# Optimization experiments

Measured on AMD Instinct MI355X. Metric: run time of the kernel, lower is better.

Reference implementation:

```python
import jax, jax.numpy as jnp
import numpy as np

SCORE_THRESHOLD = 0.5
IOU_THRESHOLD = 0.5
N = 8192
IMG = 640.0


def setup_inputs() -> dict:
    key = jax.random.key(0)
    k1, k2, k3 = jax.random.split(key, 3)
    # valid xyxy boxes on a 640px canvas: x2 > x1, y2 > y1
    xy1 = jax.random.uniform(k1, (N, 2), dtype=jnp.float32) * (IMG - 64.0)
    wh = jax.random.uniform(k2, (N, 2), dtype=jnp.float32) * 96.0 + 4.0
    xyxy = jnp.concatenate([xy1, xy1 + wh], axis=1)  # [N,4]
    person_conf = jax.random.uniform(k3, (N,), dtype=jnp.float32)  # [N]
    return {"xyxy": xyxy, "person_conf": person_conf}


def _pairwise_iou(boxes):
    # boxes: [N,4] xyxy -> iou: [N,N]
    x1, y1, x2, y2 = boxes[:, 0], boxes[:, 1], boxes[:, 2], boxes[:, 3]
    area = (x2 - x1) * (y2 - y1)  # [N]
    ix1 = jnp.maximum(x1[:, None], x1[None, :])
    iy1 = jnp.maximum(y1[:, None], y1[None, :])
    ix2 = jnp.minimum(x2[:, None], x2[None, :])
    iy2 = jnp.minimum(y2[:, None], y2[None, :])
    iw = jnp.maximum(ix2 - ix1, 0.0)
    ih = jnp.maximum(iy2 - iy1, 0.0)
    inter = iw * ih
    union = area[:, None] + area[None, :] - inter
    return inter / jnp.maximum(union, 1e-9)


def reference(xyxy, person_conf):
    # score-threshold filter (as a mask to stay jit-compatible / fixed shape)
    valid = person_conf >= SCORE_THRESHOLD  # [N]
    # sort by score descending; invalid boxes sink to the bottom
    sort_scores = jnp.where(valid, person_conf, -jnp.inf)
    order = jnp.argsort(-sort_scores)  # [N]
    boxes_s = xyxy[order]              # [N,4]
    scores_s = person_conf[order]      # [N]
    valid_s = valid[order]             # [N]

    iou = _pairwise_iou(boxes_s)  # [N,N]
    idx = jnp.arange(N)

    def body(i, keep):
        # box i (if still kept) suppresses lower-scored overlapping boxes
        sup = keep[i] & (iou[i] > IOU_THRESHOLD) & (idx > i)
        return keep & ~sup

    keep = jax.lax.fori_loop(0, N, body, valid_s)  # [N] bool

    boxes_and_scores = jnp.concatenate([boxes_s, scores_s[:, None]], axis=1)  # [N,5]
    out = jnp.where(keep[:, None], boxes_and_scores, 0.0)  # suppressed rows zeroed
    return out, keep
```

## Files before the change

kernel.cpp:

```cpp
#include <hip/hip_runtime.h>

typedef unsigned long long u64;
typedef unsigned int u32;

static constexpr int N = 8192;
static constexpr int NW = N / 64;
static constexpr int CAPE = 12288;
static constexpr int EPT = CAPE / 1024;


__device__ __forceinline__ u64 make_key(float s, int i) {
  u32 adj = (s >= 0.5f) ? (__float_as_uint(s) + 1u) : 0u;
  return ((u64)adj << 32) | (u64)(u32)(N - 1 - i);
}

__global__ __launch_bounds__(256)
void rank_kernel(const float* __restrict__ conf, u32* __restrict__ rank_partial) {
  __shared__ u64 sk[1024];
  const int t = threadIdx.x;
  const int jb = blockIdx.y;
  for (int k = t; k < 1024; k += 256) {
    int j = jb * 1024 + k;
    sk[k] = make_key(conf[j], j);
  }
  __syncthreads();
  const int i = blockIdx.x * 256 + t;
  const u64 ki = make_key(conf[i], i);
  int cnt = 0;
  #pragma unroll 8
  for (int k = 0; k < 1024; ++k) cnt += (sk[k] > ki);
  rank_partial[jb * N + i] = (u32)cnt;
}

__global__ __launch_bounds__(256)
void scatter_kernel(const float4* __restrict__ xyxy, const float* __restrict__ conf,
                    const u32* __restrict__ rank_partial,
                    float4* __restrict__ boxes_s, float* __restrict__ scores_s,
                    float* __restrict__ areas_s, int* __restrict__ ecount) {
  #pragma clang fp contract(off)
  const int i = blockIdx.x * 256 + threadIdx.x;
  if (i == 0) *ecount = 0;
  u32 r = 0;
  #pragma unroll
  for (int jb = 0; jb < 8; ++jb) r += rank_partial[jb * N + i];
  float4 b = xyxy[i];
  boxes_s[r] = b;
  scores_s[r] = conf[i];
  areas_s[r] = (b.z - b.x) * (b.w - b.y);
}

__global__ __launch_bounds__(256)
void mask_kernel(const float4* __restrict__ boxes_s, const float* __restrict__ areas_s,
                 const float* __restrict__ scores_s,
                 u64* __restrict__ edgeW, u32* __restrict__ edgeM,
                 int* __restrict__ ecount) {
  #pragma clang fp contract(off)
  __shared__ float4 cb[4][64];
  __shared__ float ca[4][64];
  const int wave = threadIdx.x >> 6;
  const int t = threadIdx.x & 63;
  const int xb = blockIdx.x * 4 + wave;
  const int yb = blockIdx.y;
  if (xb < yb) return;
  if (scores_s[xb * 64] < 0.5f) return;
  cb[wave][t] = boxes_s[xb * 64 + t];
  ca[wave][t] = areas_s[xb * 64 + t];
  const int i = yb * 64 + t;
  const float4 rb = boxes_s[i];
  const float ra = areas_s[i];
  const float sc_i = scores_s[i];
  const int jbase = xb * 64;
  u64 w = 0;
  for (int q = 0; q < 64; ++q) {
    float4 c = cb[wave][q];
    float ix1 = fmaxf(rb.x, c.x);
    float iy1 = fmaxf(rb.y, c.y);
    float ix2 = fminf(rb.z, c.z);
    float iy2 = fminf(rb.w, c.w);
    float iw = fmaxf(ix2 - ix1, 0.0f);
    float ih = fmaxf(iy2 - iy1, 0.0f);
    float inter = iw * ih;
    float uni = fmaxf((ra + ca[wave][q]) - inter, 1e-9f);
    float iou = inter / uni;
    if ((iou > 0.5f) && (jbase + q > i)) w |= (1ull << q);
  }
  if (sc_i < 0.5f) w = 0;
  u64 nz = __ballot(w != 0ull);
  if (!nz) return;
  int base = 0;
  if (t == 0) base = atomicAdd(ecount, __popcll(nz));
  base = __shfl(base, 0);
  if (w) {
    int idx = base + __popcll(nz & ((1ull << t) - 1ull));
    if (idx < CAPE) {
      edgeW[idx] = w;
      edgeM[idx] = (u32)i | ((u32)xb << 16);
    }
  }
}

__global__ __launch_bounds__(1024)
void reduce_write_kernel(const u64* __restrict__ edgeW, const u32* __restrict__ edgeM,
                         const int* __restrict__ ecount,
                         const float* __restrict__ scores_s,
                         const float4* __restrict__ boxes_s,
                         float* __restrict__ out) {
  __shared__ u32 removed32[2 * NW];
  __shared__ u32 keep32[2 * NW];
  __shared__ u64 validm[NW];
  __shared__ int chg[2];
  const int tid = threadIdx.x;
  const int lane = tid & 63;

  if (tid == 0) { chg[0] = 0; chg[1] = 0; }
  for (int p = tid; p < N; p += 1024) {
    u64 b = __ballot(scores_s[p] >= 0.5f);
    if (lane == 0) validm[p >> 6] = b;
  }
  int E = *ecount;
  if (E > CAPE) E = CAPE;

  u64 ew[EPT]; u32 em[EPT]; int ne = 0;
  #pragma unroll
  for (int k = 0; k < EPT; ++k) {
    int e = tid + k * 1024;
    if (e < E) { ew[k] = edgeW[e]; em[k] = edgeM[e]; ne = k + 1; }
    else       { ew[k] = 0; em[k] = 0; }
  }
  __syncthreads();
  if (tid < 256) keep32[tid] = ((const u32*)validm)[tid];
  __syncthreads();

  for (int it = 0; it < N; ++it) {
    if (tid < 256) removed32[tid] = 0;
    if (tid == 0) chg[(it + 1) & 1] = 0;
    __syncthreads();
    #pragma unroll
    for (int k = 0; k < EPT; ++k) {
      if (k < ne) {
        int row = em[k] & 0xffff;
        if ((keep32[row >> 5] >> (row & 31)) & 1u) {
          int x = em[k] >> 16;
          atomicOr(&removed32[2 * x],     (u32)ew[k]);
          atomicOr(&removed32[2 * x + 1], (u32)(ew[k] >> 32));
        }
      }
    }
    __syncthreads();
    if (tid < 256) {
      u32 nk = ((const u32*)validm)[tid] & ~removed32[tid];
      if (nk != keep32[tid]) { keep32[tid] = nk; chg[it & 1] = 1; }
    }
    __syncthreads();
    if (!chg[it & 1]) break;
  }

  for (int s = tid; s < N; s += 1024) {
    bool keep = (keep32[s >> 5] >> (s & 31)) & 1u;
    float4 b = boxes_s[s];
    float sc = scores_s[s];
    float* row = out + (u64)s * 5;
    if (keep) {
      row[0] = b.x; row[1] = b.y; row[2] = b.z; row[3] = b.w; row[4] = sc;
      out[N * 5 + s] = 1.0f;
    } else {
      row[0] = 0.0f; row[1] = 0.0f; row[2] = 0.0f; row[3] = 0.0f; row[4] = 0.0f;
      out[N * 5 + s] = 0.0f;
    }
  }
}

extern "C" void kernel_launch(void* const* d_in, const int* in_sizes, int n_in,
                              void* d_out, int out_size, void* d_ws, size_t ws_size,
                              hipStream_t stream) {
  const float4* xyxy = (const float4*)d_in[0];
  const float* conf  = (const float*)d_in[1];
  char* ws = (char*)d_ws;
  float4* boxes_s   = (float4*)(ws + 0);
  float*  scores_s  = (float*)(ws + 131072);
  float*  areas_s   = (float*)(ws + 163840);
  int*    ecount    = (int*)(ws + 196608);
  u64*    edgeW     = (u64*)(ws + 196672);
  u32*    edgeM     = (u32*)(ws + 294976);
  u32*    rank_partial = (u32*)(ws + 344128);
  float*  out       = (float*)d_out;

  dim3 rg(N / 256, 8);
  rank_kernel<<<rg, 256, 0, stream>>>(conf, rank_partial);
  scatter_kernel<<<N / 256, 256, 0, stream>>>(xyxy, conf, rank_partial,
                                              boxes_s, scores_s, areas_s, ecount);
  dim3 mg(NW / 4, NW);
  mask_kernel<<<mg, 256, 0, stream>>>(boxes_s, areas_s, scores_s,
                                      edgeW, edgeM, ecount);
  reduce_write_kernel<<<1, 1024, 0, stream>>>(edgeW, edgeM, ecount,
                                              scores_s, boxes_s, out);
}
```

Before: 116.2 us.

## Fuse rank+scatter and mask+reduce kernels using last-block completion counter

Merges the rank and scatter kernels into one kernel that computes the full rank per element, using 1024 threads and a shared-memory atomic sum. Merges the mask kernel with the single-block fixed-point reduction: every block builds its edges, then a global done counter elects the last finishing block to run the reduction and write the output. This cuts the launch count from four to two and drops the rank_partial buffer round trip. The cost is larger 1024-thread blocks for the mask stage, which may lower occupancy, plus threadfence and atomic overhead. The last-block pattern also depends on correct memory ordering.

```diff
diff --git a/kernel.cpp b/kernel.cpp
--- a/kernel.cpp
+++ b/kernel.cpp
@@ -14,110 +14,117 @@
   return ((u64)adj << 32) | (u64)(u32)(N - 1 - i);
 }
 
-__global__ __launch_bounds__(256)
-void rank_kernel(const float* __restrict__ conf, u32* __restrict__ rank_partial) {
-  __shared__ u64 sk[1024];
-  const int t = threadIdx.x;
-  const int jb = blockIdx.y;
-  for (int k = t; k < 1024; k += 256) {
-    int j = jb * 1024 + k;
-    sk[k] = make_key(conf[j], j);
-  }
-  __syncthreads();
-  const int i = blockIdx.x * 256 + t;
+__global__ __launch_bounds__(1024)
+void rank_scatter_kernel(const float4* __restrict__ xyxy, const float* __restrict__ conf,
+                         float4* __restrict__ boxes_s, float* __restrict__ scores_s,
+                         float* __restrict__ areas_s,
+                         int* __restrict__ ecount, int* __restrict__ done) {
+  #pragma clang fp contract(off)
+  __shared__ u64 sk[2048];
+  __shared__ u32 cnt[256];
+  const int tid = threadIdx.x;
+  const int il = tid & 255;
+  const int jq = tid >> 8;
+  const int i = blockIdx.x * 256 + il;
+  if (tid < 256) cnt[tid] = 0;
+  if (blockIdx.x == 0 && tid == 0) { *ecount = 0; *done = 0; }
   const u64 ki = make_key(conf[i], i);
-  int cnt = 0;
-  #pragma unroll 8
-  for (int k = 0; k < 1024; ++k) cnt += (sk[k] > ki);
-  rank_partial[jb * N + i] = (u32)cnt;
-}
-
-__global__ __launch_bounds__(256)
-void scatter_kernel(const float4* __restrict__ xyxy, const float* __restrict__ conf,
-                    const u32* __restrict__ rank_partial,
-                    float4* __restrict__ boxes_s, float* __restrict__ scores_s,
-                    float* __restrict__ areas_s, int* __restrict__ ecount) {
+  u32 local = 0;
+  for (int tile = 0; tile < 4; ++tile) {
+    __syncthreads();
+    int j0 = tile * 2048 + tid;
+    sk[tid] = make_key(conf[j0], j0);
+    int j1 = j0 + 1024;
+    sk[1024 + tid] = make_key(conf[j1], j1);
+    __syncthreads();
+    const int base = jq * 512;
+    #pragma unroll 8
+    for (int k = 0; k < 512; ++k) local += (sk[base + k] > ki);
+  }
+  atomicAdd(&cnt[il], local);
+  __syncthreads();
+  if (tid < 256) {
+    u32 r = cnt[tid];
+    float4 b = xyxy[i];
+    boxes_s[r] = b;
+    scores_s[r] = conf[i];
+    areas_s[r] = (b.z - b.x) * (b.w - b.y);
+  }
+}
+
+__global__ __launch_bounds__(1024)
+void mask_reduce_kernel(const float4* __restrict__ boxes_s,
+                        const float* __restrict__ areas_s,
+                        const float* __restrict__ scores_s,
+                        u64* __restrict__ edgeW, u32* __restrict__ edgeM,
+                        int* __restrict__ ecount, int* __restrict__ done,
+                        float* __restrict__ out) {
   #pragma clang fp contract(off)
-  const int i = blockIdx.x * 256 + threadIdx.x;
-  if (i == 0) *ecount = 0;
-  u32 r = 0;
-  #pragma unroll
-  for (int jb = 0; jb < 8; ++jb) r += rank_partial[jb * N + i];
-  float4 b = xyxy[i];
-  boxes_s[r] = b;
-  scores_s[r] = conf[i];
-  areas_s[r] = (b.z - b.x) * (b.w - b.y);
-}
-
-__global__ __launch_bounds__(256)
-void mask_kernel(const float4* __restrict__ boxes_s, const float* __restrict__ areas_s,
-                 const float* __restrict__ scores_s,
-                 u64* __restrict__ edgeW, u32* __restrict__ edgeM,
-                 int* __restrict__ ecount) {
-  #pragma clang fp contract(off)
-  __shared__ float4 cb[4][64];
-  __shared__ float ca[4][64];
-  const int wave = threadIdx.x >> 6;
-  const int t = threadIdx.x & 63;
-  const int xb = blockIdx.x * 4 + wave;
-  const int yb = blockIdx.y;
-  if (xb < yb) return;
-  if (scores_s[xb * 64] < 0.5f) return;
-  cb[wave][t] = boxes_s[xb * 64 + t];
-  ca[wave][t] = areas_s[xb * 64 + t];
-  const int i = yb * 64 + t;
-  const float4 rb = boxes_s[i];
-  const float ra = areas_s[i];
-  const float sc_i = scores_s[i];
-  const int jbase = xb * 64;
-  u64 w = 0;
-  for (int q = 0; q < 64; ++q) {
-    float4 c = cb[wave][q];
-    float ix1 = fmaxf(rb.x, c.x);
-    float iy1 = fmaxf(rb.y, c.y);
-    float ix2 = fminf(rb.z, c.z);
-    float iy2 = fminf(rb.w, c.w);
-    float iw = fmaxf(ix2 - ix1, 0.0f);
-    float ih = fmaxf(iy2 - iy1, 0.0f);
-    float inter = iw * ih;
-    float uni = fmaxf((ra + ca[wave][q]) - inter, 1e-9f);
-    float iou = inter / uni;
-    if ((iou > 0.5f) && (jbase + q > i)) w |= (1ull << q);
-  }
-  if (sc_i < 0.5f) w = 0;
-  u64 nz = __ballot(w != 0ull);
-  if (!nz) return;
-  int base = 0;
-  if (t == 0) base = atomicAdd(ecount, __popcll(nz));
-  base = __shfl(base, 0);
-  if (w) {
-    int idx = base + __popcll(nz & ((1ull << t) - 1ull));
-    if (idx < CAPE) {
-      edgeW[idx] = w;
-      edgeM[idx] = (u32)i | ((u32)xb << 16);
-    }
-  }
-}
-
-__global__ __launch_bounds__(1024)
-void reduce_write_kernel(const u64* __restrict__ edgeW, const u32* __restrict__ edgeM,
-                         const int* __restrict__ ecount,
-                         const float* __restrict__ scores_s,
-                         const float4* __restrict__ boxes_s,
-                         float* __restrict__ out) {
+  __shared__ float4 cb[16][64];
+  __shared__ float  ca[16][64];
   __shared__ u32 removed32[2 * NW];
   __shared__ u32 keep32[2 * NW];
   __shared__ u64 validm[NW];
   __shared__ int chg[2];
+  __shared__ int lastsh;
   const int tid = threadIdx.x;
   const int lane = tid & 63;
+  const int wave = tid >> 6;
+  const int xb = blockIdx.x * 16 + wave;
+  const int yb = blockIdx.y;
+
+  if (xb >= yb && scores_s[xb * 64] >= 0.5f) {
+    cb[wave][lane] = boxes_s[xb * 64 + lane];
+    ca[wave][lane] = areas_s[xb * 64 + lane];
+    const int i = yb * 64 + lane;
+    const float4 rb = boxes_s[i];
+    const float ra = areas_s[i];
+    const float sc_i = scores_s[i];
+    const int jbase = xb * 64;
+    u64 w = 0;
+    for (int q = 0; q < 64; ++q) {
+      float4 c = cb[wave][q];
+      float ix1 = fmaxf(rb.x, c.x);
+      float iy1 = fmaxf(rb.y, c.y);
+      float ix2 = fminf(rb.z, c.z);
+      float iy2 = fminf(rb.w, c.w);
+      float iw = fmaxf(ix2 - ix1, 0.0f);
+      float ih = fmaxf(iy2 - iy1, 0.0f);
+      float inter = iw * ih;
+      float uni = fmaxf((ra + ca[wave][q]) - inter, 1e-9f);
+      float iou = inter / uni;
+      if ((iou > 0.5f) && (jbase + q > i)) w |= (1ull << q);
+    }
+    if (sc_i < 0.5f) w = 0;
+    u64 nz = __ballot(w != 0ull);
+    if (nz) {
+      int base = 0;
+      if (lane == 0) base = atomicAdd(ecount, __popcll(nz));
+      base = __shfl(base, 0);
+      if (w) {
+        int idx = base + __popcll(nz & ((1ull << lane) - 1ull));
+        if (idx < CAPE) {
+          edgeW[idx] = w;
+          edgeM[idx] = (u32)i | ((u32)xb << 16);
+        }
+      }
+    }
+  }
+
+  __threadfence();
+  __syncthreads();
+  if (tid == 0)
+    lastsh = (atomicAdd(done, 1) == (int)(gridDim.x * gridDim.y) - 1);
+  __syncthreads();
+  if (!lastsh) return;
+  __threadfence();
 
   if (tid == 0) { chg[0] = 0; chg[1] = 0; }
   for (int p = tid; p < N; p += 1024) {
     u64 b = __ballot(scores_s[p] >= 0.5f);
     if (lane == 0) validm[p >> 6] = b;
   }
-  int E = *ecount;
+  int E = atomicAdd(ecount, 0);
   if (E > CAPE) E = CAPE;
 
   u64 ew[EPT]; u32 em[EPT]; int ne = 0;
@@ -180,18 +187,15 @@
   float*  scores_s  = (float*)(ws + 131072);
   float*  areas_s   = (float*)(ws + 163840);
   int*    ecount    = (int*)(ws + 196608);
+  int*    done      = (int*)(ws + 196612);
   u64*    edgeW     = (u64*)(ws + 196672);
   u32*    edgeM     = (u32*)(ws + 294976);
-  u32*    rank_partial = (u32*)(ws + 344128);
   float*  out       = (float*)d_out;
 
-  dim3 rg(N / 256, 8);
-  rank_kernel<<<rg, 256, 0, stream>>>(conf, rank_partial);
-  scatter_kernel<<<N / 256, 256, 0, stream>>>(xyxy, conf, rank_partial,
-                                              boxes_s, scores_s, areas_s, ecount);
-  dim3 mg(NW / 4, NW);
-  mask_kernel<<<mg, 256, 0, stream>>>(boxes_s, areas_s, scores_s,
-                                      edgeW, edgeM, ecount);
-  reduce_write_kernel<<<1, 1024, 0, stream>>>(edgeW, edgeM, ecount,
-                                              scores_s, boxes_s, out);
-}
+  rank_scatter_kernel<<<N / 256, 1024, 0, stream>>>(xyxy, conf, boxes_s,
+                                                    scores_s, areas_s,
+                                                    ecount, done);
+  dim3 mg(NW / 16, NW);
+  mask_reduce_kernel<<<mg, 1024, 0, stream>>>(boxes_s, areas_s, scores_s,
+                                              edgeW, edgeM, ecount, done, out);
+}
```

After: 367.0 us. +215.8%, slower.
